# Kernel tuning notes

Hardware: AMD Instinct MI355X
Metric: run time of the kernel (lower is better)

Reference implementation:

```python
import jax, jax.numpy as jnp
import numpy as np

D = 4096      # model dim
H = 32        # query heads (== kv heads; GQA path in source is buggy, default is MHA)
HD = D // H   # head_dim = 128
BASE = 10000.0


def _rope_cos_sin(S):
    # inv_freq over half the head dim, duplicated to full head_dim (standard RoPE)
    inv_freq = 1.0 / (BASE ** (jnp.arange(0, HD, 2, dtype=jnp.float32) / HD))
    t = jnp.arange(S, dtype=jnp.float32)
    freqs = jnp.outer(t, inv_freq)                      # [S, HD//2]
    cos = jnp.concatenate([jnp.cos(freqs)] * 2, axis=-1)  # [S, HD]
    sin = jnp.concatenate([jnp.sin(freqs)] * 2, axis=-1)
    return cos[None, None], sin[None, None]             # [1,1,S,HD]


def _rotate_half(x):
    x1, x2 = jnp.split(x, 2, axis=-1)
    return jnp.concatenate((-x2, x1), axis=-1)


def setup_inputs() -> dict:
    key = jax.random.key(0)
    ks = jax.random.split(key, 5)
    B, S = 2, 2048
    x = jax.random.normal(ks[0], (B, S, D), dtype=jnp.float32)
    # causal mask: 1 = attend, 0 = masked
    mask = jnp.tril(jnp.ones((S, S), dtype=bool))[None, None]  # [1,1,S,S]
    w = lambda k: jax.random.normal(k, (D, D), dtype=jnp.float32) * 0.02
    return {"x": x, "mask": mask, "Wq": w(ks[1]), "Wk": w(ks[2]), "Wv": w(ks[3]), "Wo": w(ks[4])}


def reference(x, mask, Wq, Wk, Wv, Wo):
    B, S, _ = x.shape
    scale = HD ** -0.5
    # torch nn.Linear: y = x @ W.T
    q = (x @ Wq.T).reshape(B, S, H, HD).transpose(0, 2, 1, 3)  # [B,H,S,HD]
    k = (x @ Wk.T).reshape(B, S, H, HD).transpose(0, 2, 1, 3)
    v = (x @ Wv.T).reshape(B, S, H, HD).transpose(0, 2, 1, 3)
    cos, sin = _rope_cos_sin(S)
    q = q * cos + _rotate_half(q) * sin
    k = k * cos + _rotate_half(k) * sin
    scores = jnp.einsum('bhqd,bhkd->bhqk', q, k) * scale       # [B,H,S,S]
    scores = jnp.where(mask, scores, jnp.float32(-10000.0))
    probs = jax.nn.softmax(scores, axis=-1)                    # dropout p=0.0
    ctx = jnp.einsum('bhqk,bhkd->bhqd', probs, v)
    ctx = ctx.transpose(0, 2, 1, 3).reshape(B, S, H * HD)      # [B,S,D]
    return ctx @ Wo.T
```

## Files before the change

### kernel.cpp

```cpp
#include <hip/hip_runtime.h>

typedef __bf16 bf16x8 __attribute__((ext_vector_type(8)));
typedef float  f32x4  __attribute__((ext_vector_type(4)));
typedef unsigned short ushort8v __attribute__((ext_vector_type(8)));

#define DEV __device__ __forceinline__

constexpr int Dm = 4096;
constexpr int Sq = 2048;
constexpr int Bb = 2;
constexpr int Hh = 32;
constexpr int HDd = 128;

DEV unsigned short f2bf(float f) {
  union { float f; unsigned u; } v; v.f = f;
  unsigned u = v.u;
  return (unsigned short)((u + 0x7fffu + ((u >> 16) & 1u)) >> 16);
}
DEV float bf2f(unsigned short s) {
  union { unsigned u; float f; } v; v.u = ((unsigned)s) << 16;
  return v.f;
}

__global__ __launch_bounds__(256) void cast_f32_bf16(const float* __restrict__ src,
                                                     unsigned short* __restrict__ dst,
                                                     int n8) {
  int i = blockIdx.x * 256 + threadIdx.x;
  if (i >= n8) return;
  const float4* s4 = (const float4*)src;
  float4 a = s4[2 * i], b = s4[2 * i + 1];
  ushort8v o;
  o[0] = f2bf(a.x); o[1] = f2bf(a.y); o[2] = f2bf(a.z); o[3] = f2bf(a.w);
  o[4] = f2bf(b.x); o[5] = f2bf(b.y); o[6] = f2bf(b.z); o[7] = f2bf(b.w);
  *(ushort8v*)(dst + 8 * i) = o;
}

__global__ __launch_bounds__(256) void rope_tables(float* __restrict__ cosT,
                                                   float* __restrict__ sinT) {
  int idx = blockIdx.x * 256 + threadIdx.x;
  int s = idx >> 6, i = idx & 63;
  float inv = expf(-(float)i * (9.210340371976184f / 64.0f));
  float f = (float)s * inv;
  cosT[idx] = cosf(f);
  sinT[idx] = sinf(f);
}

template <int WF32>
__global__ __launch_bounds__(256) void gemm_nt(const unsigned short* __restrict__ A,
                                               const unsigned short* __restrict__ Bw,
                                               unsigned short* __restrict__ Cb,
                                               float* __restrict__ Cf, int K) {
  constexpr int TM = 128, BK = 64;
  __shared__ unsigned short lA[TM * BK];
  __shared__ unsigned short lB[TM * BK];
  const int tid = threadIdx.x;
  const int l = tid & 63, w = tid >> 6;
  const int wm = (w >> 1) * 64, wn = (w & 1) * 64;
  const int m0 = blockIdx.x * TM, n0 = blockIdx.y * TM;
  f32x4 acc[4][4] = {};

  const unsigned short* Ag = A + (size_t)m0 * K;
  const unsigned short* Bg = Bw + (size_t)n0 * K;
  const int srow = l >> 3;
  const int scb = (l & 7) * 16;

  for (int k0 = 0; k0 < K; k0 += BK) {
    __syncthreads();
#pragma unroll
    for (int i = 0; i < 4; i++) {
      int row = w * 32 + i * 8 + srow;
      __builtin_amdgcn_global_load_lds(
          (const __attribute__((address_space(1))) void*)((const char*)Ag +
              ((size_t)row * K + k0) * 2 + scb),
          (__attribute__((address_space(3))) void*)(lA + (w * 4 + i) * 512),
          16, 0, 0);
      __builtin_amdgcn_global_load_lds(
          (const __attribute__((address_space(1))) void*)((const char*)Bg +
              ((size_t)row * K + k0) * 2 + scb),
          (__attribute__((address_space(3))) void*)(lB + (w * 4 + i) * 512),
          16, 0, 0);
    }
    __syncthreads();
#pragma unroll
    for (int kc = 0; kc < 2; kc++) {
      bf16x8 af[4], bfr[4];
#pragma unroll
      for (int mi = 0; mi < 4; mi++)
        af[mi] = *(const bf16x8*)((const char*)lA +
                                  (wm + mi * 16 + (l & 15)) * 128 + kc * 64 + (l >> 4) * 16);
#pragma unroll
      for (int ni = 0; ni < 4; ni++)
        bfr[ni] = *(const bf16x8*)((const char*)lB +
                                   (wn + ni * 16 + (l & 15)) * 128 + kc * 64 + (l >> 4) * 16);
#pragma unroll
      for (int mi = 0; mi < 4; mi++)
#pragma unroll
        for (int ni = 0; ni < 4; ni++)
          acc[mi][ni] = __builtin_amdgcn_mfma_f32_16x16x32_bf16(af[mi], bfr[ni], acc[mi][ni], 0, 0, 0);
    }
  }
#pragma unroll
  for (int mi = 0; mi < 4; mi++) {
    int mrow = m0 + wm + mi * 16 + (l >> 4) * 4;
#pragma unroll
    for (int ni = 0; ni < 4; ni++) {
      int ncol = n0 + wn + ni * 16 + (l & 15);
#pragma unroll
      for (int r = 0; r < 4; r++) {
        if constexpr (WF32)
          Cf[(size_t)(mrow + r) * Dm + ncol] = acc[mi][ni][r];
        else
          Cb[(size_t)(mrow + r) * Dm + ncol] = f2bf(acc[mi][ni][r]);
      }
    }
  }
}

__global__ __launch_bounds__(256) void rope_apply(unsigned short* __restrict__ Q,
                                                  unsigned short* __restrict__ Kt,
                                                  const float* __restrict__ cosT,
                                                  const float* __restrict__ sinT) {
  int idx = blockIdx.x * 256 + threadIdx.x;
  unsigned short* P = blockIdx.y ? Kt : Q;
  int j = idx & 7;
  int h = (idx >> 3) & 31;
  int m = idx >> 8;
  int s = m & (Sq - 1);
  size_t base = (size_t)m * Dm + h * HDd + j * 8;
  ushort8v u1 = *(ushort8v*)(P + base);
  ushort8v u2 = *(ushort8v*)(P + base + 64);
  const float* cp = cosT + s * 64 + j * 8;
  const float* sp = sinT + s * 64 + j * 8;
  ushort8v o1, o2;
#pragma unroll
  for (int e = 0; e < 8; e++) {
    float c = cp[e], sn = sp[e];
    float x1 = bf2f(u1[e]), x2 = bf2f(u2[e]);
    o1[e] = f2bf(x1 * c - x2 * sn);
    o2[e] = f2bf(x2 * c + x1 * sn);
  }
  *(ushort8v*)(P + base) = o1;
  *(ushort8v*)(P + base + 64) = o2;
}

__global__ __launch_bounds__(256) void transpose_v(const unsigned short* __restrict__ V,
                                                   unsigned short* __restrict__ VT) {
  __shared__ unsigned short t[32][33];
  int bh = blockIdx.z;
  int s0 = blockIdx.x * 32, d0 = blockIdx.y * 32;
  int tx = threadIdx.x, ty = threadIdx.y;
  int b = bh >> 5, h = bh & 31;
#pragma unroll
  for (int i = 0; i < 4; i++) {
    int row = ty + i * 8;
    t[row][tx] = V[((size_t)(b * Sq + s0 + row)) * Dm + h * HDd + d0 + tx];
  }
  __syncthreads();
#pragma unroll
  for (int i = 0; i < 4; i++) {
    int row = ty + i * 8;
    VT[((size_t)bh * HDd + d0 + row) * Sq + s0 + tx] = t[tx][row];
  }
}

__global__ __launch_bounds__(512) void flash_attn(const unsigned short* __restrict__ Qg,
                                                  const unsigned short* __restrict__ Kg,
                                                  const unsigned short* __restrict__ VTg,
                                                  unsigned short* __restrict__ Ctx) {
  constexpr int PP = 72;
  __shared__ unsigned short lK[64 * 128];
  __shared__ unsigned short lV[128 * 64];
  __shared__ unsigned short lP[8][16 * PP];
  const int tid = threadIdx.x, l = tid & 63, w = tid >> 6;
  const int qb = gridDim.x - 1 - blockIdx.x;
  const int q0 = qb * 128;
  const int bh = blockIdx.y, b = bh >> 5, h = bh & 31;
  const int ntile = 2 * qb + 2;

  bf16x8 qf[4];
  {
    int qrow = q0 + w * 16 + (l & 15);
    const unsigned short* qp = Qg + ((size_t)(b * Sq + qrow)) * Dm + h * HDd + (l >> 4) * 8;
#pragma unroll
    for (int c = 0; c < 4; c++) qf[c] = *(const bf16x8*)(qp + c * 32);
  }

  f32x4 acc[8] = {};
  float mrun[4] = {-1e30f, -1e30f, -1e30f, -1e30f};
  float lrun[4] = {0.f, 0.f, 0.f, 0.f};
  const float scale = 0.08838834764831845f;
  const float L2E = 1.4426950408889634f;

  const int kr0 = tid >> 4;
  const int kcb = (tid & 15) * 16;
  const int vr0 = tid >> 3;
  const int vcb = (tid & 7) * 16;
  const char* Kbase = (const char*)Kg + ((size_t)(b * Sq) * Dm + h * HDd) * 2;
  const char* Vbase = (const char*)VTg + ((size_t)bh * HDd) * Sq * 2;
  uint4 kreg0, kreg1, vreg0, vreg1;

  auto LOADT = [&](int kv0) {
    kreg0 = *(const uint4*)(Kbase + (size_t)(kv0 + kr0) * (Dm * 2) + kcb);
    kreg1 = *(const uint4*)(Kbase + (size_t)(kv0 + kr0 + 32) * (Dm * 2) + kcb);
    vreg0 = *(const uint4*)(Vbase + (size_t)vr0 * (Sq * 2) + kv0 * 2 + vcb);
    vreg1 = *(const uint4*)(Vbase + (size_t)(vr0 + 64) * (Sq * 2) + kv0 * 2 + vcb);
  };
  auto STORET = [&]() {
    int ks = kcb ^ ((kr0 & 7) << 4);
    int vs = vcb ^ ((vr0 & 7) << 4);
    *(uint4*)((char*)lK + kr0 * 256 + ks) = kreg0;
    *(uint4*)((char*)lK + (kr0 + 32) * 256 + ks) = kreg1;
    *(uint4*)((char*)lV + vr0 * 128 + vs) = vreg0;
    *(uint4*)((char*)lV + (vr0 + 64) * 128 + vs) = vreg1;
  };

  LOADT(0);
  STORET();
  __syncthreads();

  for (int t = 0; t < ntile; t++) {
    const int kv0 = t * 64;
    if (t + 1 < ntile) LOADT((t + 1) * 64);

    f32x4 sc[4] = {};
    __builtin_amdgcn_s_setprio(1);
#pragma unroll
    for (int nb = 0; nb < 4; nb++) {
      int kvr = nb * 16 + (l & 15);
#pragma unroll
      for (int c = 0; c < 4; c++) {
        int cb = (c * 64 + (l >> 4) * 16) ^ ((kvr & 7) << 4);
        bf16x8 kf = *(const bf16x8*)((const char*)lK + kvr * 256 + cb);
        sc[nb] = __builtin_amdgcn_mfma_f32_16x16x32_bf16(qf[c], kf, sc[nb], 0, 0, 0);
      }
    }
    __builtin_amdgcn_s_setprio(0);

    float sv[4][4];
    const bool domask = (t >= ntile - 2);
#pragma unroll
    for (int nb = 0; nb < 4; nb++) {
      int kvg = kv0 + nb * 16 + (l & 15);
#pragma unroll
      for (int r = 0; r < 4; r++) {
        float vv = sc[nb][r] * scale;
        if (domask) {
          int qg = q0 + w * 16 + (l >> 4) * 4 + r;
          vv = (kvg <= qg) ? vv : -1e30f;
        }
        sv[nb][r] = vv;
      }
    }
    float rmax[4];
#pragma unroll
    for (int r = 0; r < 4; r++)
      rmax[r] = fmaxf(fmaxf(sv[0][r], sv[1][r]), fmaxf(sv[2][r], sv[3][r]));
#pragma unroll
    for (int d = 1; d < 16; d <<= 1)
#pragma unroll
      for (int r = 0; r < 4; r++) rmax[r] = fmaxf(rmax[r], __shfl_xor(rmax[r], d, 64));

    float mnew[4], alpha[4], psum[4];
#pragma unroll
    for (int r = 0; r < 4; r++) {
      mnew[r] = fmaxf(mrun[r], rmax[r]);
      alpha[r] = exp2f((mrun[r] - mnew[r]) * L2E);
      psum[r] = 0.f;
    }
#pragma unroll
    for (int nb = 0; nb < 4; nb++)
#pragma unroll
      for (int r = 0; r < 4; r++) {
        float pe = exp2f((sv[nb][r] - mnew[r]) * L2E);
        sv[nb][r] = pe;
        psum[r] += pe;
      }
#pragma unroll
    for (int d = 1; d < 16; d <<= 1)
#pragma unroll
      for (int r = 0; r < 4; r++) psum[r] += __shfl_xor(psum[r], d, 64);
#pragma unroll
    for (int r = 0; r < 4; r++) {
      lrun[r] = lrun[r] * alpha[r] + psum[r];
      mrun[r] = mnew[r];
    }
#pragma unroll
    for (int hdnb = 0; hdnb < 8; hdnb++)
#pragma unroll
      for (int r = 0; r < 4; r++) acc[hdnb][r] *= alpha[r];

    unsigned short* P = lP[w];
#pragma unroll
    for (int nb = 0; nb < 4; nb++)
#pragma unroll
      for (int r = 0; r < 4; r++)
        P[((l >> 4) * 4 + r) * PP + nb * 16 + (l & 15)] = f2bf(sv[nb][r]);

    bf16x8 pf[2];
#pragma unroll
    for (int kc = 0; kc < 2; kc++)
      pf[kc] = *(const bf16x8*)(P + (l & 15) * PP + kc * 32 + (l >> 4) * 8);
    __builtin_amdgcn_s_setprio(1);
#pragma unroll
    for (int hdnb = 0; hdnb < 8; hdnb++) {
      int hdr = hdnb * 16 + (l & 15);
#pragma unroll
      for (int kc = 0; kc < 2; kc++) {
        int cb = (kc * 64 + (l >> 4) * 16) ^ ((hdr & 7) << 4);
        bf16x8 vf = *(const bf16x8*)((const char*)lV + hdr * 128 + cb);
        acc[hdnb] = __builtin_amdgcn_mfma_f32_16x16x32_bf16(pf[kc], vf, acc[hdnb], 0, 0, 0);
      }
    }
    __builtin_amdgcn_s_setprio(0);

    __syncthreads();
    if (t + 1 < ntile) STORET();
    __syncthreads();
  }

  float invl[4];
#pragma unroll
  for (int r = 0; r < 4; r++) invl[r] = 1.0f / lrun[r];
#pragma unroll
  for (int hdnb = 0; hdnb < 8; hdnb++)
#pragma unroll
    for (int r = 0; r < 4; r++) {
      size_t mrow = (size_t)(b * Sq + q0 + w * 16 + (l >> 4) * 4 + r);
      Ctx[mrow * Dm + h * HDd + hdnb * 16 + (l & 15)] = f2bf(acc[hdnb][r] * invl[r]);
    }
}

extern "C" void kernel_launch(void* const* d_in, const int* in_sizes, int n_in,
                              void* d_out, int out_size, void* d_ws, size_t ws_size,
                              hipStream_t stream) {
  (void)in_sizes; (void)n_in; (void)out_size; (void)ws_size;
  const float* x  = (const float*)d_in[0];
  const float* Wq = (const float*)d_in[2];
  const float* Wk = (const float*)d_in[3];
  const float* Wv = (const float*)d_in[4];
  const float* Wo = (const float*)d_in[5];
  float* out = (float*)d_out;

  char* p = (char*)d_ws;
  const size_t TB = (size_t)Dm * Dm * 2;
  unsigned short* xb = (unsigned short*)p; p += TB;
  unsigned short* wq = (unsigned short*)p; p += TB;
  unsigned short* wk = (unsigned short*)p; p += TB;
  unsigned short* wv = (unsigned short*)p; p += TB;
  unsigned short* wo = (unsigned short*)p; p += TB;
  unsigned short* qb = (unsigned short*)p; p += TB;
  unsigned short* kb = (unsigned short*)p; p += TB;
  unsigned short* vb = (unsigned short*)p; p += TB;
  float* cosT = (float*)p; p += (size_t)Sq * 64 * 4;
  float* sinT = (float*)p; p += (size_t)Sq * 64 * 4;
  unsigned short* vT  = xb;
  unsigned short* ctx = vb;

  const int n8 = Dm * Dm / 8;
  const int castBlocks = n8 / 256;

  cast_f32_bf16<<<castBlocks, 256, 0, stream>>>(x, xb, n8);
  cast_f32_bf16<<<castBlocks, 256, 0, stream>>>(Wq, wq, n8);
  cast_f32_bf16<<<castBlocks, 256, 0, stream>>>(Wk, wk, n8);
  cast_f32_bf16<<<castBlocks, 256, 0, stream>>>(Wv, wv, n8);
  cast_f32_bf16<<<castBlocks, 256, 0, stream>>>(Wo, wo, n8);
  rope_tables<<<512, 256, 0, stream>>>(cosT, sinT);

  dim3 gg(32, 32);
  gemm_nt<0><<<gg, 256, 0, stream>>>(xb, wq, qb, nullptr, Dm);
  gemm_nt<0><<<gg, 256, 0, stream>>>(xb, wk, kb, nullptr, Dm);
  gemm_nt<0><<<gg, 256, 0, stream>>>(xb, wv, vb, nullptr, Dm);

  rope_apply<<<dim3(4096, 2), 256, 0, stream>>>(qb, kb, cosT, sinT);
  transpose_v<<<dim3(64, 4, 64), dim3(32, 8), 0, stream>>>(vb, vT);

  flash_attn<<<dim3(Sq / 128, Bb * Hh), 512, 0, stream>>>(qb, kb, vT, ctx);

  gemm_nt<1><<<gg, 256, 0, stream>>>(ctx, wo, nullptr, out, Dm);
}
```

Measured before the change: 1.547 ms.

## Double-buffer flash attention, pair causal q-blocks, defer softmax rescale, vectorize V transpose

```diff
diff --git a/kernel.cpp b/kernel.cpp
--- a/kernel.cpp
+++ b/kernel.cpp
@@ -13,9 +13,9 @@
 constexpr int HDd = 128;
 
 DEV unsigned short f2bf(float f) {
-  union { float f; unsigned u; } v; v.f = f;
-  unsigned u = v.u;
-  return (unsigned short)((u + 0x7fffu + ((u >> 16) & 1u)) >> 16);
+  __bf16 h = (__bf16)f;
+  union { __bf16 h; unsigned short u; } v; v.h = h;
+  return v.u;
 }
 DEV float bf2f(unsigned short s) {
   union { unsigned u; float f; } v; v.u = ((unsigned)s) << 16;
@@ -145,51 +145,43 @@
 
 __global__ __launch_bounds__(256) void transpose_v(const unsigned short* __restrict__ V,
                                                    unsigned short* __restrict__ VT) {
-  __shared__ unsigned short t[32][33];
-  int bh = blockIdx.z;
-  int s0 = blockIdx.x * 32, d0 = blockIdx.y * 32;
-  int tx = threadIdx.x, ty = threadIdx.y;
-  int b = bh >> 5, h = bh & 31;
+  __shared__ unsigned short t[64][130];
+  const int tid = threadIdx.x;
+  const int s0 = blockIdx.x * 64;
+  const int bh = blockIdx.y;
+  const int b = bh >> 5, h = bh & 31;
+  const int lhd = (tid & 15) * 8, ls = tid >> 4;
 #pragma unroll
   for (int i = 0; i < 4; i++) {
-    int row = ty + i * 8;
-    t[row][tx] = V[((size_t)(b * Sq + s0 + row)) * Dm + h * HDd + d0 + tx];
+    int s = ls + i * 16;
+    ushort8v v = *(const ushort8v*)(V + ((size_t)(b * Sq + s0 + s)) * Dm + h * HDd + lhd);
+    *(ushort8v*)&t[s][lhd] = v;
   }
   __syncthreads();
-#pragma unroll
-  for (int i = 0; i < 4; i++) {
-    int row = ty + i * 8;
-    VT[((size_t)bh * HDd + d0 + row) * Sq + s0 + tx] = t[tx][row];
-  }
-}
-
-__global__ __launch_bounds__(512) void flash_attn(const unsigned short* __restrict__ Qg,
-                                                  const unsigned short* __restrict__ Kg,
-                                                  const unsigned short* __restrict__ VTg,
-                                                  unsigned short* __restrict__ Ctx) {
-  constexpr int PP = 72;
-  __shared__ unsigned short lK[64 * 128];
-  __shared__ unsigned short lV[128 * 64];
-  __shared__ unsigned short lP[8][16 * PP];
+  const int osc = (tid & 7) * 8, ohd = tid >> 3;
+#pragma unroll
+  for (int j = 0; j < 4; j++) {
+    int hd = ohd + j * 32;
+    ushort8v o;
+#pragma unroll
+    for (int e = 0; e < 8; e++) o[e] = t[osc + e][hd];
+    *(ushort8v*)(VT + ((size_t)(bh * HDd + hd)) * Sq + s0 + osc) = o;
+  }
+}
+
+__global__ __launch_bounds__(512, 4) void flash_attn(const unsigned short* __restrict__ Qg,
+                                                     const unsigned short* __restrict__ Kg,
+                                                     const unsigned short* __restrict__ VTg,
+                                                     unsigned short* __restrict__ Ctx) {
+  __shared__ unsigned short lK[2][64 * 128];
+  __shared__ unsigned short lV[2][128 * 64];
+  __shared__ unsigned short lP[8][16 * 64];
   const int tid = threadIdx.x, l = tid & 63, w = tid >> 6;
-  const int qb = gridDim.x - 1 - blockIdx.x;
-  const int q0 = qb * 128;
+  const int bx = blockIdx.x;
   const int bh = blockIdx.y, b = bh >> 5, h = bh & 31;
-  const int ntile = 2 * qb + 2;
-
-  bf16x8 qf[4];
-  {
-    int qrow = q0 + w * 16 + (l & 15);
-    const unsigned short* qp = Qg + ((size_t)(b * Sq + qrow)) * Dm + h * HDd + (l >> 4) * 8;
-#pragma unroll
-    for (int c = 0; c < 4; c++) qf[c] = *(const bf16x8*)(qp + c * 32);
-  }
-
-  f32x4 acc[8] = {};
-  float mrun[4] = {-1e30f, -1e30f, -1e30f, -1e30f};
-  float lrun[4] = {0.f, 0.f, 0.f, 0.f};
-  const float scale = 0.08838834764831845f;
-  const float L2E = 1.4426950408889634f;
+
+  const float SC = 0.12755102331353136f;
+  const float THR = 11.541560327111707f;
 
   const int kr0 = tid >> 4;
   const int kcb = (tid & 15) * 16;
@@ -198,6 +190,8 @@
   const char* Kbase = (const char*)Kg + ((size_t)(b * Sq) * Dm + h * HDd) * 2;
   const char* Vbase = (const char*)VTg + ((size_t)bh * HDd) * Sq * 2;
   uint4 kreg0, kreg1, vreg0, vreg1;
+  const int ks = kcb ^ ((kr0 & 7) << 4);
+  const int vs = vcb ^ ((vr0 & 7) << 4);
 
   auto LOADT = [&](int kv0) {
     kreg0 = *(const uint4*)(Kbase + (size_t)(kv0 + kr0) * (Dm * 2) + kcb);
@@ -205,129 +199,160 @@
     vreg0 = *(const uint4*)(Vbase + (size_t)vr0 * (Sq * 2) + kv0 * 2 + vcb);
     vreg1 = *(const uint4*)(Vbase + (size_t)(vr0 + 64) * (Sq * 2) + kv0 * 2 + vcb);
   };
-  auto STORET = [&]() {
-    int ks = kcb ^ ((kr0 & 7) << 4);
-    int vs = vcb ^ ((vr0 & 7) << 4);
-    *(uint4*)((char*)lK + kr0 * 256 + ks) = kreg0;
-    *(uint4*)((char*)lK + (kr0 + 32) * 256 + ks) = kreg1;
-    *(uint4*)((char*)lV + vr0 * 128 + vs) = vreg0;
-    *(uint4*)((char*)lV + (vr0 + 64) * 128 + vs) = vreg1;
+  auto STORET = [&](int buf) {
+    *(uint4*)((char*)lK[buf] + kr0 * 256 + ks) = kreg0;
+    *(uint4*)((char*)lK[buf] + (kr0 + 32) * 256 + ks) = kreg1;
+    *(uint4*)((char*)lV[buf] + vr0 * 128 + vs) = vreg0;
+    *(uint4*)((char*)lV[buf] + (vr0 + 64) * 128 + vs) = vreg1;
   };
 
-  LOADT(0);
-  STORET();
-  __syncthreads();
-
-  for (int t = 0; t < ntile; t++) {
-    const int kv0 = t * 64;
-    if (t + 1 < ntile) LOADT((t + 1) * 64);
-
-    f32x4 sc[4] = {};
-    __builtin_amdgcn_s_setprio(1);
-#pragma unroll
-    for (int nb = 0; nb < 4; nb++) {
-      int kvr = nb * 16 + (l & 15);
-#pragma unroll
-      for (int c = 0; c < 4; c++) {
-        int cb = (c * 64 + (l >> 4) * 16) ^ ((kvr & 7) << 4);
-        bf16x8 kf = *(const bf16x8*)((const char*)lK + kvr * 256 + cb);
-        sc[nb] = __builtin_amdgcn_mfma_f32_16x16x32_bf16(qf[c], kf, sc[nb], 0, 0, 0);
-      }
+  for (int part = 0; part < 2; ++part) {
+    const int qb = part ? bx : (15 - bx);
+    const int q0 = qb * 128;
+    const int ntile = 2 * qb + 2;
+
+    bf16x8 qf[4];
+    {
+      int qrow = q0 + w * 16 + (l & 15);
+      const unsigned short* qp = Qg + ((size_t)(b * Sq + qrow)) * Dm + h * HDd + (l >> 4) * 8;
+#pragma unroll
+      for (int c = 0; c < 4; c++) qf[c] = *(const bf16x8*)(qp + c * 32);
     }
-    __builtin_amdgcn_s_setprio(0);
-
-    float sv[4][4];
-    const bool domask = (t >= ntile - 2);
-#pragma unroll
-    for (int nb = 0; nb < 4; nb++) {
-      int kvg = kv0 + nb * 16 + (l & 15);
+
+    f32x4 acc[8] = {};
+    float mrun[4] = {-1e30f, -1e30f, -1e30f, -1e30f};
+    float lrun[4] = {0.f, 0.f, 0.f, 0.f};
+
+    LOADT(0);
+    STORET(0);
+    if (ntile > 1) LOADT(64);
+    __syncthreads();
+
+    int cur = 0;
+    for (int t = 0; t < ntile; t++) {
+      if (t + 1 < ntile) STORET(cur ^ 1);
+      if (t + 2 < ntile) LOADT((t + 2) * 64);
+
+      const char* Kl = (const char*)lK[cur];
+      const char* Vl = (const char*)lV[cur];
+      const int kv0 = t * 64;
+
+      f32x4 sc[4] = {};
+      __builtin_amdgcn_s_setprio(1);
+#pragma unroll
+      for (int nb = 0; nb < 4; nb++) {
+        int kvr = nb * 16 + (l & 15);
+#pragma unroll
+        for (int c = 0; c < 4; c++) {
+          int cb = (c * 64 + (l >> 4) * 16) ^ ((kvr & 7) << 4);
+          bf16x8 kf = *(const bf16x8*)(Kl + kvr * 256 + cb);
+          sc[nb] = __builtin_amdgcn_mfma_f32_16x16x32_bf16(qf[c], kf, sc[nb], 0, 0, 0);
+        }
+      }
+      __builtin_amdgcn_s_setprio(0);
+
+      const bool domask = (t >= ntile - 2);
+#pragma unroll
+      for (int nb = 0; nb < 4; nb++) {
+        int kvg = kv0 + nb * 16 + (l & 15);
+#pragma unroll
+        for (int r = 0; r < 4; r++) {
+          float vv = sc[nb][r] * SC;
+          if (domask) {
+            int qg = q0 + w * 16 + (l >> 4) * 4 + r;
+            vv = (kvg <= qg) ? vv : -1e30f;
+          }
+          sc[nb][r] = vv;
+        }
+      }
+      float rmax[4];
+#pragma unroll
+      for (int r = 0; r < 4; r++)
+        rmax[r] = fmaxf(fmaxf(sc[0][r], sc[1][r]), fmaxf(sc[2][r], sc[3][r]));
+#pragma unroll
+      for (int d = 1; d < 16; d <<= 1)
+#pragma unroll
+        for (int r = 0; r < 4; r++) rmax[r] = fmaxf(rmax[r], __shfl_xor(rmax[r], d, 64));
+
+      bool defer = __all((rmax[0] - mrun[0] <= THR) & (rmax[1] - mrun[1] <= THR) &
+                         (rmax[2] - mrun[2] <= THR) & (rmax[3] - mrun[3] <= THR));
+      if (!defer) {
+        float alpha[4];
+#pragma unroll
+        for (int r = 0; r < 4; r++) {
+          float mnew = fmaxf(mrun[r], rmax[r]);
+          alpha[r] = exp2f(mrun[r] - mnew);
+          mrun[r] = mnew;
+        }
+#pragma unroll
+        for (int hdnb = 0; hdnb < 8; hdnb++)
+#pragma unroll
+          for (int r = 0; r < 4; r++) acc[hdnb][r] *= alpha[r];
+#pragma unroll
+        for (int r = 0; r < 4; r++) lrun[r] *= alpha[r];
+      }
+
+      float psum[4] = {0.f, 0.f, 0.f, 0.f};
+#pragma unroll
+      for (int nb = 0; nb < 4; nb++)
+#pragma unroll
+        for (int r = 0; r < 4; r++) {
+          float pe = exp2f(sc[nb][r] - mrun[r]);
+          sc[nb][r] = pe;
+          psum[r] += pe;
+        }
+#pragma unroll
+      for (int d = 1; d < 16; d <<= 1)
+#pragma unroll
+        for (int r = 0; r < 4; r++) psum[r] += __shfl_xor(psum[r], d, 64);
+#pragma unroll
+      for (int r = 0; r < 4; r++) lrun[r] += psum[r];
+
+      char* P = (char*)lP[w];
+#pragma unroll
+      for (int nb = 0; nb < 4; nb++)
+#pragma unroll
+        for (int r = 0; r < 4; r++) {
+          int prow = (l >> 4) * 4 + r;
+          int pb = (prow * 128 + nb * 32 + (l & 15) * 2) ^ ((prow & 7) << 4);
+          *(unsigned short*)(P + pb) = f2bf(sc[nb][r]);
+        }
+
+      bf16x8 pf[2];
+#pragma unroll
+      for (int kc = 0; kc < 2; kc++) {
+        int row = l & 15;
+        int pb = row * 128 + ((kc * 64 + (l >> 4) * 16) ^ ((row & 7) << 4));
+        pf[kc] = *(const bf16x8*)(P + pb);
+      }
+      __builtin_amdgcn_s_setprio(1);
+#pragma unroll
+      for (int hdnb = 0; hdnb < 8; hdnb++) {
+        int hdr = hdnb * 16 + (l & 15);
+#pragma unroll
+        for (int kc = 0; kc < 2; kc++) {
+          int cb = (kc * 64 + (l >> 4) * 16) ^ ((hdr & 7) << 4);
+          bf16x8 vf = *(const bf16x8*)(Vl + hdr * 128 + cb);
+          acc[hdnb] = __builtin_amdgcn_mfma_f32_16x16x32_bf16(pf[kc], vf, acc[hdnb], 0, 0, 0);
+        }
+      }
+      __builtin_amdgcn_s_setprio(0);
+
+      __syncthreads();
+      cur ^= 1;
+    }
+
+    float invl[4];
+#pragma unroll
+    for (int r = 0; r < 4; r++) invl[r] = 1.0f / lrun[r];
+#pragma unroll
+    for (int hdnb = 0; hdnb < 8; hdnb++)
 #pragma unroll
       for (int r = 0; r < 4; r++) {
-        float vv = sc[nb][r] * scale;
-        if (domask) {
-          int qg = q0 + w * 16 + (l >> 4) * 4 + r;
-          vv = (kvg <= qg) ? vv : -1e30f;
-        }
-        sv[nb][r] = vv;
-      }
-    }
-    float rmax[4];
-#pragma unroll
-    for (int r = 0; r < 4; r++)
-      rmax[r] = fmaxf(fmaxf(sv[0][r], sv[1][r]), fmaxf(sv[2][r], sv[3][r]));
-#pragma unroll
-    for (int d = 1; d < 16; d <<= 1)
-#pragma unroll
-      for (int r = 0; r < 4; r++) rmax[r] = fmaxf(rmax[r], __shfl_xor(rmax[r], d, 64));
-
-    float mnew[4], alpha[4], psum[4];
-#pragma unroll
-    for (int r = 0; r < 4; r++) {
-      mnew[r] = fmaxf(mrun[r], rmax[r]);
-      alpha[r] = exp2f((mrun[r] - mnew[r]) * L2E);
-      psum[r] = 0.f;
-    }
-#pragma unroll
-    for (int nb = 0; nb < 4; nb++)
-#pragma unroll
-      for (int r = 0; r < 4; r++) {
-        float pe = exp2f((sv[nb][r] - mnew[r]) * L2E);
-        sv[nb][r] = pe;
-        psum[r] += pe;
-      }
-#pragma unroll
-    for (int d = 1; d < 16; d <<= 1)
-#pragma unroll
-      for (int r = 0; r < 4; r++) psum[r] += __shfl_xor(psum[r], d, 64);
-#pragma unroll
-    for (int r = 0; r < 4; r++) {
-      lrun[r] = lrun[r] * alpha[r] + psum[r];
-      mrun[r] = mnew[r];
-    }
-#pragma unroll
-    for (int hdnb = 0; hdnb < 8; hdnb++)
-#pragma unroll
-      for (int r = 0; r < 4; r++) acc[hdnb][r] *= alpha[r];
-
-    unsigned short* P = lP[w];
-#pragma unroll
-    for (int nb = 0; nb < 4; nb++)
-#pragma unroll
-      for (int r = 0; r < 4; r++)
-        P[((l >> 4) * 4 + r) * PP + nb * 16 + (l & 15)] = f2bf(sv[nb][r]);
-
-    bf16x8 pf[2];
-#pragma unroll
-    for (int kc = 0; kc < 2; kc++)
-      pf[kc] = *(const bf16x8*)(P + (l & 15) * PP + kc * 32 + (l >> 4) * 8);
-    __builtin_amdgcn_s_setprio(1);
-#pragma unroll
-    for (int hdnb = 0; hdnb < 8; hdnb++) {
-      int hdr = hdnb * 16 + (l & 15);
-#pragma unroll
-      for (int kc = 0; kc < 2; kc++) {
-        int cb = (kc * 64 + (l >> 4) * 16) ^ ((hdr & 7) << 4);
-        bf16x8 vf = *(const bf16x8*)((const char*)lV + hdr * 128 + cb);
-        acc[hdnb] = __builtin_amdgcn_mfma_f32_16x16x32_bf16(pf[kc], vf, acc[hdnb], 0, 0, 0);
-      }
-    }
-    __builtin_amdgcn_s_setprio(0);
-
-    __syncthreads();
-    if (t + 1 < ntile) STORET();
-    __syncthreads();
-  }
-
-  float invl[4];
-#pragma unroll
-  for (int r = 0; r < 4; r++) invl[r] = 1.0f / lrun[r];
-#pragma unroll
-  for (int hdnb = 0; hdnb < 8; hdnb++)
-#pragma unroll
-    for (int r = 0; r < 4; r++) {
-      size_t mrow = (size_t)(b * Sq + q0 + w * 16 + (l >> 4) * 4 + r);
-      Ctx[mrow * Dm + h * HDd + hdnb * 16 + (l & 15)] = f2bf(acc[hdnb][r] * invl[r]);
-    }
+        size_t mrow = (size_t)(b * Sq + q0 + w * 16 + (l >> 4) * 4 + r);
+        Ctx[mrow * Dm + h * HDd + hdnb * 16 + (l & 15)] = f2bf(acc[hdnb][r] * invl[r]);
+      }
+  }
 }
 
 extern "C" void kernel_launch(void* const* d_in, const int* in_sizes, int n_in,
@@ -372,9 +397,9 @@
   gemm_nt<0><<<gg, 256, 0, stream>>>(xb, wv, vb, nullptr, Dm);
 
   rope_apply<<<dim3(4096, 2), 256, 0, stream>>>(qb, kb, cosT, sinT);
-  transpose_v<<<dim3(64, 4, 64), dim3(32, 8), 0, stream>>>(vb, vT);
-
-  flash_attn<<<dim3(Sq / 128, Bb * Hh), 512, 0, stream>>>(qb, kb, vT, ctx);
+  transpose_v<<<dim3(32, 64), 256, 0, stream>>>(vb, vT);
+
+  flash_attn<<<dim3(8, Bb * Hh), 512, 0, stream>>>(qb, kb, vT, ctx);
 
   gemm_nt<1><<<gg, 256, 0, stream>>>(ctx, wo, nullptr, out, Dm);
 }
```

Result: faster. 1.374 ms (-11.2%).
